# Optimization experiments

Hardware: AMD Instinct MI355X
Metric: run time of the kernel (lower is better)

The kernel has to match this reference:

```python
import jax, jax.numpy as jnp
import numpy as np

N_USERS = 100000
N_MOVIES = 20000
N_EDGES = 600000
FEAT = 64
HID = 128
OUT = 64
N_TUPLES = 100000


def _sage(x_src, x_dst, src_idx, dst_idx, n_dst, Wl, bl, Wr):
    # PyG SAGEConv (mean aggr): lin_l(mean of gathered src feats) + lin_r(x_dst)
    msg = x_src[src_idx]                                        # [E, d_src]
    summ = jax.ops.segment_sum(msg, dst_idx, num_segments=n_dst)
    cnt = jax.ops.segment_sum(jnp.ones((src_idx.shape[0],), x_src.dtype),
                              dst_idx, num_segments=n_dst)
    mean = summ / jnp.maximum(cnt, 1.0)[:, None]
    return mean @ Wl.T + bl + x_dst @ Wr.T


def setup_inputs() -> dict:
    key = jax.random.key(0)
    ks = jax.random.split(key, 20)
    s = 0.05
    return {
        "movie_x": jax.random.normal(ks[0], (N_MOVIES, FEAT), jnp.float32),
        "user_idx": jax.random.randint(ks[1], (N_EDGES,), 0, N_USERS),
        "movie_idx": jax.random.randint(ks[2], (N_EDGES,), 0, N_MOVIES),
        "tuples_coo": jax.random.randint(ks[3], (2, N_TUPLES), 0, N_MOVIES),
        "user_emb": jax.random.normal(ks[4], (1, HID), jnp.float32) * s,
        "W1l": jax.random.normal(ks[5], (HID, FEAT), jnp.float32) * s,
        "b1": jnp.zeros((HID,), jnp.float32),
        "W1r": jax.random.normal(ks[6], (HID, HID), jnp.float32) * s,
        "W2l": jax.random.normal(ks[7], (HID, HID), jnp.float32) * s,
        "b2": jnp.zeros((HID,), jnp.float32),
        "W2r": jax.random.normal(ks[8], (HID, FEAT), jnp.float32) * s,
        "W3l": jax.random.normal(ks[9], (HID, HID), jnp.float32) * s,
        "b3": jnp.zeros((HID,), jnp.float32),
        "W3r": jax.random.normal(ks[10], (HID, HID), jnp.float32) * s,
        "Wlin1": jax.random.normal(ks[11], (OUT, HID), jnp.float32) * s,
        "blin1": jnp.zeros((OUT,), jnp.float32),
        "Wlin2": jax.random.normal(ks[12], (OUT, HID), jnp.float32) * s,
        "blin2": jnp.zeros((OUT,), jnp.float32),
    }


def reference(movie_x, user_idx, movie_idx, tuples_coo, user_emb,
              W1l, b1, W1r, W2l, b2, W2r, W3l, b3, W3r,
              Wlin1, blin1, Wlin2, blin2):
    n_users = N_USERS
    user_x0 = jnp.broadcast_to(user_emb, (n_users, HID))  # emb.weight.repeat
    # conv1: (movie -> user) rev_rates edges: src=movie_idx, dst=user_idx
    user_x = jax.nn.relu(_sage(movie_x, user_x0, movie_idx, user_idx, n_users, W1l, b1, W1r))
    # conv2: (user -> movie) rates edges: src=user_idx, dst=movie_idx
    movie_z = jax.nn.relu(_sage(user_x, movie_x, user_idx, movie_idx, N_MOVIES, W2l, b2, W2r))
    # conv3: (movie -> user) again
    user_z = jax.nn.relu(_sage(movie_z, user_x, movie_idx, user_idx, n_users, W3l, b3, W3r))
    z_user = user_z @ Wlin1.T + blin1
    z_movie = movie_z @ Wlin2.T + blin2
    X = jnp.vstack((z_user, z_movie))
    # relation_schema = ['user', 'movie']: offset movie indices by n_users
    new_index = jnp.vstack((tuples_coo[0], tuples_coo[1] + n_users))
    return X, new_index
```

## Files before the change

### kernel.cpp

```cpp
#include <hip/hip_runtime.h>

typedef __attribute__((ext_vector_type(8))) short short8;
typedef __attribute__((ext_vector_type(4))) float f32x4;

static const int NU = 100000;
static const int NM = 20000;
static const int NE = 600000;
static const int FEAT = 64;
static const int HID = 128;
static const int OUTD = 64;
static const int NTOT = NU + NM;
static const int NLIST = 2 * NE;
static const int CVT_TOT = 81920 + NM * FEAT;
static const int CVT_BLKS = (CVT_TOT + 255) / 256;
static const int IDX_BLKS = (100000 + 255) / 256;

static const int UB_SHIFT = 9;
static const int MB_SHIFT = 7;
static const int NBU = (NU + 511) >> 9;
static const int NBM = (NM + 127) >> 7;
static const int NBUCK = NBU + NBM;
static const int EPB = 4096;
static const int NPBLK = (NE + EPB - 1) / EPB;

__device__ inline float b2f(unsigned short h) {
    unsigned int u = ((unsigned int)h) << 16;
    float f; __builtin_memcpy(&f, &u, 4); return f;
}
__device__ inline unsigned short f2b(float f) {
    unsigned int u; __builtin_memcpy(&u, &f, 4);
    u += 0x7FFFu + ((u >> 16) & 1u);
    return (unsigned short)(u >> 16);
}
__device__ inline unsigned int pk2(float a, float b) {
    return (unsigned int)f2b(a) | ((unsigned int)f2b(b) << 16);
}
__device__ inline int wswz(int row, int bc, int rowbytes) {
    return row * rowbytes + (bc ^ ((row & 7) << 4));
}

__global__ __launch_bounds__(256) void k_hist_misc(
        const int* __restrict__ ui, const int* __restrict__ mi, int* __restrict__ ghist,
        const float* __restrict__ w1l, const float* __restrict__ w2l,
        const float* __restrict__ w2r, const float* __restrict__ w3l,
        const float* __restrict__ w3r, const float* __restrict__ wl1,
        const float* __restrict__ wl2, const float* __restrict__ mx,
        unsigned short* __restrict__ dst,
        const int* __restrict__ tpl, float* __restrict__ oidx,
        const float* __restrict__ ue, const float* __restrict__ w1r,
        const float* __restrict__ b1, float* __restrict__ c1) {
    __shared__ int h[NBUCK];
    const int b = blockIdx.x;
    const int tid = threadIdx.x;
    if (b < NPBLK) {
        for (int i = tid; i < NBUCK; i += 256) h[i] = 0;
        __syncthreads();
#pragma unroll
        for (int it = 0; it < EPB / 256; ++it) {
            int e = b * EPB + it * 256 + tid;
            if (e < NE) {
                atomicAdd(&h[ui[e] >> UB_SHIFT], 1);
                atomicAdd(&h[NBU + (mi[e] >> MB_SHIFT)], 1);
            }
        }
        __syncthreads();
        for (int i = tid; i < NBUCK; i += 256)
            if (h[i]) atomicAdd(&ghist[i], h[i]);
    } else if (b < NPBLK + CVT_BLKS) {
        int g = (b - NPBLK) * 256 + tid;
        if (g >= CVT_TOT) return;
        const float* s; int o;
        if      (g < 8192)   { s = w1l; o = g; }
        else if (g < 24576)  { s = w2l; o = g - 8192; }
        else if (g < 32768)  { s = w2r; o = g - 24576; }
        else if (g < 49152)  { s = w3l; o = g - 32768; }
        else if (g < 65536)  { s = w3r; o = g - 49152; }
        else if (g < 73728)  { s = wl1; o = g - 65536; }
        else if (g < 81920)  { s = wl2; o = g - 73728; }
        else                 { s = mx;  o = g - 81920; }
        dst[g] = f2b(s[o]);
    } else if (b < NPBLK + CVT_BLKS + IDX_BLKS) {
        int i = (b - NPBLK - CVT_BLKS) * 256 + tid;
        if (i < 100000) {
            oidx[i] = (float)tpl[i];
            oidx[100000 + i] = (float)(tpl[100000 + i] + NU);
        }
    } else {
        int hh = tid;
        if (hh < HID) {
            float a = 0.f;
#pragma unroll 16
            for (int k = 0; k < HID; ++k) a += ue[k] * w1r[hh * HID + k];
            c1[hh] = a + b1[hh];
        }
    }
}

__global__ __launch_bounds__(512) void k_bscan(const int* __restrict__ ghist,
                                               int* __restrict__ bb,
                                               int* __restrict__ gcur) {
    __shared__ int s[512];
    const int tid = threadIdx.x;
    int v = (tid < NBUCK) ? ghist[tid] : 0;
    s[tid] = v;
    __syncthreads();
#pragma unroll
    for (int off = 1; off < 512; off <<= 1) {
        int x = (tid >= off) ? s[tid - off] : 0;
        __syncthreads();
        s[tid] += x;
        __syncthreads();
    }
    int excl = s[tid] - v;
    if (tid < NBUCK) { bb[tid] = excl; gcur[tid] = excl; }
    if (tid == 511) bb[NBUCK] = s[511];
}

__global__ __launch_bounds__(256) void k_part(const int* __restrict__ ui,
                                              const int* __restrict__ mi,
                                              int* __restrict__ gcur,
                                              int* __restrict__ entries) {
    __shared__ int h[NBUCK], base[NBUCK], cur[NBUCK];
    const int tid = threadIdx.x;
    for (int i = tid; i < NBUCK; i += 256) h[i] = 0;
    __syncthreads();

    int eu[EPB / 256], em[EPB / 256];
#pragma unroll
    for (int it = 0; it < EPB / 256; ++it) {
        int e = blockIdx.x * EPB + it * 256 + tid;
        if (e < NE) {
            eu[it] = ui[e]; em[it] = mi[e];
            atomicAdd(&h[eu[it] >> UB_SHIFT], 1);
            atomicAdd(&h[NBU + (em[it] >> MB_SHIFT)], 1);
        } else eu[it] = -1;
    }
    __syncthreads();
    for (int i = tid; i < NBUCK; i += 256) {
        int c = h[i];
        base[i] = c ? atomicAdd(&gcur[i], c) : 0;
        cur[i] = 0;
    }
    __syncthreads();
#pragma unroll
    for (int it = 0; it < EPB / 256; ++it) {
        if (eu[it] < 0) continue;
        int u = eu[it], m = em[it];
        int bu = u >> UB_SHIFT;
        int o1 = base[bu] + atomicAdd(&cur[bu], 1);
        entries[o1] = (m << UB_SHIFT) | (u & 511);
        int bm = NBU + (m >> MB_SHIFT);
        int o2 = base[bm] + atomicAdd(&cur[bm], 1);
        entries[o2] = (u << MB_SHIFT) | (m & 127);
    }
}

__global__ __launch_bounds__(256) void k_csr(const int* __restrict__ bb,
                                             const int* __restrict__ entries,
                                             int* __restrict__ rp,
                                             int* __restrict__ list) {
    __shared__ int lcnt[512], lrp[512], lcur[512], ps[256];
    const int b = blockIdx.x;
    const int tid = threadIdx.x;
    const int s = bb[b], e = bb[b + 1];
    const bool isU = b < NBU;
    const int shift = isU ? UB_SHIFT : MB_SHIFT;
    const int mask = isU ? 511 : 127;
    const int n0 = isU ? (b << UB_SHIFT) : ((b - NBU) << MB_SHIFT);
    const int nNodes = isU ? min(512, NU - n0) : min(128, NM - n0);
    const int g0 = isU ? n0 : NU + n0;

    for (int i = tid; i < 512; i += 256) { lcnt[i] = 0; lcur[i] = 0; }
    __syncthreads();
    for (int i = s + tid; i < e; i += 256)
        atomicAdd(&lcnt[entries[i] & mask], 1);
    __syncthreads();
    int a0 = lcnt[2 * tid], a1 = lcnt[2 * tid + 1];
    int pr = a0 + a1;
    ps[tid] = pr;
    __syncthreads();
#pragma unroll
    for (int off = 1; off < 256; off <<= 1) {
        int x = (tid >= off) ? ps[tid - off] : 0;
        __syncthreads();
        ps[tid] += x;
        __syncthreads();
    }
    int excl = ps[tid] - pr;
    lrp[2 * tid] = excl;
    lrp[2 * tid + 1] = excl + a0;
    __syncthreads();
    for (int i = tid; i < nNodes; i += 256) rp[g0 + i] = s + lrp[i];
    if (b == NBUCK - 1 && tid == 0) rp[NTOT] = e;
    for (int i = s + tid; i < e; i += 256) {
        int p = entries[i];
        int dl = p & mask;
        int off = s + lrp[dl] + atomicAdd(&lcur[dl], 1);
        list[off] = p >> shift;
    }
}

template<int C>
__global__ __launch_bounds__(256) void k_gather_b(const unsigned short* __restrict__ src,
                                                  const int* __restrict__ rp,
                                                  const int* __restrict__ list,
                                                  unsigned short* __restrict__ dst,
                                                  int base, int n) {
    constexpr int TPN = C / 8;
    constexpr int NPB = 256 / TPN;
    const int node = blockIdx.x * NPB + threadIdx.x / TPN;
    if (node >= n) return;
    const int c8 = (threadIdx.x % TPN) * 8;
    const int g = base + node;
    const int s = rp[g], e = rp[g + 1];

    float a[8];
#pragma unroll
    for (int j = 0; j < 8; ++j) a[j] = 0.f;

    int i = s;
    for (; i + 1 < e; i += 2) {
        int r0 = list[i], r1 = list[i + 1];
        short8 v0 = *reinterpret_cast<const short8*>(src + (size_t)r0 * C + c8);
        short8 v1 = *reinterpret_cast<const short8*>(src + (size_t)r1 * C + c8);
#pragma unroll
        for (int j = 0; j < 8; ++j)
            a[j] += b2f((unsigned short)v0[j]) + b2f((unsigned short)v1[j]);
    }
    if (i < e) {
        int r0 = list[i];
        short8 v0 = *reinterpret_cast<const short8*>(src + (size_t)r0 * C + c8);
#pragma unroll
        for (int j = 0; j < 8; ++j) a[j] += b2f((unsigned short)v0[j]);
    }
    const float sc = 1.0f / (float)max(e - s, 1);
    short8 o;
#pragma unroll
    for (int j = 0; j < 8; ++j) o[j] = (short)f2b(a[j] * sc);
    *reinterpret_cast<short8*>(dst + (size_t)node * C + c8) = o;
}

__global__ __launch_bounds__(256) void k_gather_relu(const unsigned short* __restrict__ Y1,
                                                     const int* __restrict__ rp,
                                                     const int* __restrict__ list,
                                                     const float* __restrict__ c1,
                                                     unsigned short* __restrict__ user_x,
                                                     int n) {
    const int node = blockIdx.x * 16 + threadIdx.x / 16;
    if (node >= n) return;
    const int c8 = (threadIdx.x % 16) * 8;
    const int s = rp[node], e = rp[node + 1];

    float a[8];
#pragma unroll
    for (int j = 0; j < 8; ++j) a[j] = 0.f;

    int i = s;
    for (; i + 1 < e; i += 2) {
        int r0 = list[i], r1 = list[i + 1];
        short8 v0 = *reinterpret_cast<const short8*>(Y1 + (size_t)r0 * HID + c8);
        short8 v1 = *reinterpret_cast<const short8*>(Y1 + (size_t)r1 * HID + c8);
#pragma unroll
        for (int j = 0; j < 8; ++j)
            a[j] += b2f((unsigned short)v0[j]) + b2f((unsigned short)v1[j]);
    }
    if (i < e) {
        int r0 = list[i];
        short8 v0 = *reinterpret_cast<const short8*>(Y1 + (size_t)r0 * HID + c8);
#pragma unroll
        for (int j = 0; j < 8; ++j) a[j] += b2f((unsigned short)v0[j]);
    }
    const float sc = 1.0f / (float)max(e - s, 1);
    float4 cv0 = *reinterpret_cast<const float4*>(c1 + c8);
    float4 cv1 = *reinterpret_cast<const float4*>(c1 + c8 + 4);
    float r[8];
    r[0] = fmaxf(a[0] * sc + cv0.x, 0.f); r[1] = fmaxf(a[1] * sc + cv0.y, 0.f);
    r[2] = fmaxf(a[2] * sc + cv0.z, 0.f); r[3] = fmaxf(a[3] * sc + cv0.w, 0.f);
    r[4] = fmaxf(a[4] * sc + cv1.x, 0.f); r[5] = fmaxf(a[5] * sc + cv1.y, 0.f);
    r[6] = fmaxf(a[6] * sc + cv1.z, 0.f); r[7] = fmaxf(a[7] * sc + cv1.w, 0.f);
    uint4 o;
    o.x = pk2(r[0], r[1]); o.y = pk2(r[2], r[3]);
    o.z = pk2(r[4], r[5]); o.w = pk2(r[6], r[7]);
    *reinterpret_cast<uint4*>(user_x + (size_t)node * HID + c8) = o;
}

template<int K, int NO, bool AVEC, bool RELU, bool F32OUT>
__global__ __launch_bounds__(256) void k_mf2(const unsigned short* __restrict__ X,
                                             const unsigned short* __restrict__ W,
                                             const float* __restrict__ vec,
                                             void* __restrict__ Yv, int M) {
    constexpr int KT = K / 32;
    constexpr int CG = NO / 16;
    constexpr int WB = NO * K * 2;
    constexpr int RB = K * 2;
    __shared__ __align__(16) char lds[WB];
    const int tid = threadIdx.x;
    const int lane = tid & 63;
    const int wv = tid >> 6;
    const int rbase = blockIdx.x * 128 + wv * 32;
    const int lr = lane & 15;
    const int kg = lane >> 4;

#pragma unroll
    for (int i = 0; i < WB / 16 / 256; ++i) {
        int idx = tid + i * 256;
        int row = idx / (RB / 16);
        int bc = (idx % (RB / 16)) * 16;
        *reinterpret_cast<uint4*>(lds + wswz(row, bc, RB)) =
            *reinterpret_cast<const uint4*>((const char*)W + idx * 16);
    }

    short8 xb[2][KT];
#pragma unroll
    for (int t = 0; t < 2; ++t) {
        int row = min(rbase + t * 16 + lr, M - 1);
#pragma unroll
        for (int kt = 0; kt < KT; ++kt)
            xb[t][kt] = *reinterpret_cast<const short8*>(
                X + (size_t)row * K + kt * 32 + kg * 8);
    }
    __syncthreads();

    f32x4 acc[2][CG];
#pragma unroll
    for (int t = 0; t < 2; ++t)
#pragma unroll
        for (int c = 0; c < CG; ++c) acc[t][c] = (f32x4){0.f, 0.f, 0.f, 0.f};

#pragma unroll
    for (int cg = 0; cg < CG; ++cg) {
        short8 wf[KT];
#pragma unroll
        for (int kt = 0; kt < KT; ++kt)
            wf[kt] = *reinterpret_cast<const short8*>(
                lds + wswz(cg * 16 + lr, kt * 64 + kg * 16, RB));
#pragma unroll
        for (int kt = 0; kt < KT; ++kt)
#pragma unroll
            for (int t = 0; t < 2; ++t)
                acc[t][cg] = __builtin_amdgcn_mfma_f32_16x16x32_bf16(
                    wf[kt], xb[t][kt], acc[t][cg], 0, 0, 0);
    }

#pragma unroll
    for (int t = 0; t < 2; ++t) {
        const int u = rbase + t * 16 + lr;
        if (u >= M) continue;
#pragma unroll
        for (int cg = 0; cg < CG; ++cg) {
            const int h0 = cg * 16 + kg * 4;
            float v[4];
#pragma unroll
            for (int r = 0; r < 4; ++r) v[r] = acc[t][cg][r];
            if (AVEC) {
                float4 vv = *reinterpret_cast<const float4*>(vec + h0);
                v[0] += vv.x; v[1] += vv.y; v[2] += vv.z; v[3] += vv.w;
            }
            if (RELU)
#pragma unroll
                for (int r = 0; r < 4; ++r) v[r] = fmaxf(v[r], 0.f);
            if (F32OUT) {
                float4 o = make_float4(v[0], v[1], v[2], v[3]);
                *reinterpret_cast<float4*>((float*)Yv + (size_t)u * NO + h0) = o;
            } else {
                uint2 o = make_uint2(pk2(v[0], v[1]), pk2(v[2], v[3]));
                *reinterpret_cast<uint2*>((unsigned short*)Yv + (size_t)u * NO + h0) = o;
            }
        }
    }
}

__global__ __launch_bounds__(256) void k_fused_u(
        const unsigned short* __restrict__ S3, const unsigned short* __restrict__ user_x,
        const unsigned short* __restrict__ W3r, const float* __restrict__ b3,
        const unsigned short* __restrict__ Wl1, const float* __restrict__ bl1,
        float* __restrict__ out, int M) {
    __shared__ __align__(16) char lds[49152];
    const int tid = threadIdx.x;
    const int lane = tid & 63;
    const int wv = tid >> 6;
    const int rbase = blockIdx.x * 128 + wv * 32;
    const int lr = lane & 15;
    const int kg = lane >> 4;

#pragma unroll
    for (int i = 0; i < 8; ++i) {
        int idx = tid + i * 256;
        int row = idx >> 4, bc = (idx & 15) << 4;
        *reinterpret_cast<uint4*>(lds + wswz(row, bc, 256)) =
            *reinterpret_cast<const uint4*>((const char*)W3r + idx * 16);
    }
#pragma unroll
    for (int i = 0; i < 4; ++i) {
        int idx = tid + i * 256;
        int row = idx >> 4, bc = (idx & 15) << 4;
        *reinterpret_cast<uint4*>(lds + 32768 + wswz(row, bc, 256)) =
            *reinterpret_cast<const uint4*>((const char*)Wl1 + idx * 16);
    }

    short8 xc[2][4];
#pragma unroll
    for (int t = 0; t < 2; ++t) {
        int row = min(rbase + t * 16 + lr, M - 1);
#pragma unroll
        for (int kt = 0; kt < 4; ++kt)
            xc[t][kt] = *reinterpret_cast<const short8*>(
                user_x + (size_t)row * HID + kt * 32 + kg * 8);
    }
    __syncthreads();

    f32x4 acc[2][8];
#pragma unroll
    for (int t = 0; t < 2; ++t)
#pragma unroll
        for (int c = 0; c < 8; ++c) acc[t][c] = (f32x4){0.f, 0.f, 0.f, 0.f};

#pragma unroll
    for (int cg = 0; cg < 8; ++cg) {
        short8 wr[4];
#pragma unroll
        for (int kt = 0; kt < 4; ++kt)
            wr[kt] = *reinterpret_cast<const short8*>(
                lds + wswz(cg * 16 + lr, kt * 64 + kg * 16, 256));
#pragma unroll
        for (int kt = 0; kt < 4; ++kt)
#pragma unroll
            for (int t = 0; t < 2; ++t)
                acc[t][cg] = __builtin_amdgcn_mfma_f32_16x16x32_bf16(
                    wr[kt], xc[t][kt], acc[t][cg], 0, 0, 0);
    }
    __syncthreads();

#pragma unroll
    for (int t = 0; t < 2; ++t) {
        const int ul = wv * 32 + t * 16 + lr;
        const int u = min(rbase + t * 16 + lr, M - 1);
#pragma unroll
        for (int cg = 0; cg < 8; ++cg) {
            const int h0 = cg * 16 + kg * 4;
            uint2 s3 = *reinterpret_cast<const uint2*>(S3 + (size_t)u * HID + h0);
            float4 vv = *reinterpret_cast<const float4*>(b3 + h0);
            float v0 = fmaxf(acc[t][cg][0] + b2f((unsigned short)(s3.x & 0xffff)) + vv.x, 0.f);
            float v1 = fmaxf(acc[t][cg][1] + b2f((unsigned short)(s3.x >> 16)) + vv.y, 0.f);
            float v2 = fmaxf(acc[t][cg][2] + b2f((unsigned short)(s3.y & 0xffff)) + vv.z, 0.f);
            float v3 = fmaxf(acc[t][cg][3] + b2f((unsigned short)(s3.y >> 16)) + vv.w, 0.f);
            uint2 pk = make_uint2(pk2(v0, v1), pk2(v2, v3));
            *reinterpret_cast<uint2*>(lds + wswz(ul, h0 * 2, 256)) = pk;
        }
    }
    __syncthreads();

    short8 zb[2][4];
#pragma unroll
    for (int t = 0; t < 2; ++t) {
        const int ul = wv * 32 + t * 16 + lr;
#pragma unroll
        for (int kt = 0; kt < 4; ++kt)
            zb[t][kt] = *reinterpret_cast<const short8*>(
                lds + wswz(ul, kt * 64 + kg * 16, 256));
    }
    f32x4 a2[2][4];
#pragma unroll
    for (int t = 0; t < 2; ++t)
#pragma unroll
        for (int c = 0; c < 4; ++c) a2[t][c] = (f32x4){0.f, 0.f, 0.f, 0.f};
#pragma unroll
    for (int cg = 0; cg < 4; ++cg) {
        short8 wf[4];
#pragma unroll
        for (int kt = 0; kt < 4; ++kt)
            wf[kt] = *reinterpret_cast<const short8*>(
                lds + 32768 + wswz(cg * 16 + lr, kt * 64 + kg * 16, 256));
#pragma unroll
        for (int kt = 0; kt < 4; ++kt)
#pragma unroll
            for (int t = 0; t < 2; ++t)
                a2[t][cg] = __builtin_amdgcn_mfma_f32_16x16x32_bf16(
                    wf[kt], zb[t][kt], a2[t][cg], 0, 0, 0);
    }
#pragma unroll
    for (int t = 0; t < 2; ++t) {
        const int u = rbase + t * 16 + lr;
        if (u >= M) continue;
#pragma unroll
        for (int cg = 0; cg < 4; ++cg) {
            const int o0 = cg * 16 + kg * 4;
            float4 bb = *reinterpret_cast<const float4*>(bl1 + o0);
            float4 o = make_float4(a2[t][cg][0] + bb.x, a2[t][cg][1] + bb.y,
                                   a2[t][cg][2] + bb.z, a2[t][cg][3] + bb.w);
            *reinterpret_cast<float4*>(out + (size_t)u * OUTD + o0) = o;
        }
    }
}

__global__ __launch_bounds__(256) void k_fused_m(
        const unsigned short* __restrict__ mean2, const unsigned short* __restrict__ mxb,
        const unsigned short* __restrict__ W2l, const unsigned short* __restrict__ W2r,
        const float* __restrict__ b2, unsigned short* __restrict__ movie_z,
        const unsigned short* __restrict__ Wl2, const float* __restrict__ bl2,
        const unsigned short* __restrict__ W3l, unsigned short* __restrict__ Y3,
        float* __restrict__ out, int M) {
    __shared__ __align__(16) char lds[65536];
    const int tid = threadIdx.x;
    const int lane = tid & 63;
    const int wv = tid >> 6;
    const int rbase = blockIdx.x * 128 + wv * 32;
    const int lr = lane & 15;
    const int kg = lane >> 4;

#pragma unroll
    for (int i = 0; i < 8; ++i) {
        int idx = tid + i * 256;
        int row = idx >> 4, bc = (idx & 15) << 4;
        *reinterpret_cast<uint4*>(lds + wswz(row, bc, 256)) =
            *reinterpret_cast<const uint4*>((const char*)W2l + idx * 16);
    }
#pragma unroll
    for (int i = 0; i < 4; ++i) {
        int idx = tid + i * 256;
        int row = idx >> 3, bc = (idx & 7) << 4;
        *reinterpret_cast<uint4*>(lds + 32768 + wswz(row, bc, 128)) =
            *reinterpret_cast<const uint4*>((const char*)W2r + idx * 16);
        int row2 = idx >> 4, bc2 = (idx & 15) << 4;
        *reinterpret_cast<uint4*>(lds + 49152 + wswz(row2, bc2, 256)) =
            *reinterpret_cast<const uint4*>((const char*)Wl2 + idx * 16);
    }

    short8 xa[2][4], xc[2][2];
#pragma unroll
    for (int t = 0; t < 2; ++t) {
        int row = min(rbase + t * 16 + lr, M - 1);
#pragma unroll
        for (int kt = 0; kt < 4; ++kt)
            xa[t][kt] = *reinterpret_cast<const short8*>(
                mean2 + (size_t)row * HID + kt * 32 + kg * 8);
#pragma unroll
        for (int kt = 0; kt < 2; ++kt)
            xc[t][kt] = *reinterpret_cast<const short8*>(
                mxb + (size_t)row * FEAT + kt * 32 + kg * 8);
    }
    __syncthreads();

    f32x4 acc[2][8];
#pragma unroll
    for (int t = 0; t < 2; ++t)
#pragma unroll
        for (int c = 0; c < 8; ++c) acc[t][c] = (f32x4){0.f, 0.f, 0.f, 0.f};

#pragma unroll
    for (int cg = 0; cg < 8; ++cg) {
        short8 wl[4], wr[2];
#pragma unroll
        for (int kt = 0; kt < 4; ++kt)
            wl[kt] = *reinterpret_cast<const short8*>(
                lds + wswz(cg * 16 + lr, kt * 64 + kg * 16, 256));
#pragma unroll
        for (int kt = 0; kt < 2; ++kt)
            wr[kt] = *reinterpret_cast<const short8*>(
                lds + 32768 + wswz(cg * 16 + lr, kt * 64 + kg * 16, 128));
#pragma unroll
        for (int kt = 0; kt < 4; ++kt)
#pragma unroll
            for (int t = 0; t < 2; ++t)
                acc[t][cg] = __builtin_amdgcn_mfma_f32_16x16x32_bf16(
                    wl[kt], xa[t][kt], acc[t][cg], 0, 0, 0);
#pragma unroll
        for (int kt = 0; kt < 2; ++kt)
#pragma unroll
            for (int t = 0; t < 2; ++t)
                acc[t][cg] = __builtin_amdgcn_mfma_f32_16x16x32_bf16(
                    wr[kt], xc[t][kt], acc[t][cg], 0, 0, 0);
    }
    __syncthreads();

#pragma unroll
    for (int t = 0; t < 2; ++t) {
        const int ul = wv * 32 + t * 16 + lr;
        const int u = rbase + t * 16 + lr;
#pragma unroll
        for (int cg = 0; cg < 8; ++cg) {
            const int h0 = cg * 16 + kg * 4;
            float4 vv = *reinterpret_cast<const float4*>(b2 + h0);
            float v0 = fmaxf(acc[t][cg][0] + vv.x, 0.f);
            float v1 = fmaxf(acc[t][cg][1] + vv.y, 0.f);
            float v2 = fmaxf(acc[t][cg][2] + vv.z, 0.f);
            float v3 = fmaxf(acc[t][cg][3] + vv.w, 0.f);
            uint2 pk = make_uint2(pk2(v0, v1), pk2(v2, v3));
            *reinterpret_cast<uint2*>(lds + wswz(ul, h0 * 2, 256)) = pk;
            if (u < M)
                *reinterpret_cast<uint2*>(movie_z + (size_t)u * HID + h0) = pk;
        }
    }
    __syncthreads();

    short8 zb[2][4];
#pragma unroll
    for (int t = 0; t < 2; ++t) {
        const int ul = wv * 32 + t * 16 + lr;
#pragma unroll
        for (int kt = 0; kt < 4; ++kt)
            zb[t][kt] = *reinterpret_cast<const short8*>(
                lds + wswz(ul, kt * 64 + kg * 16, 256));
    }
    f32x4 a2[2][4];
#pragma unroll
    for (int t = 0; t < 2; ++t)
#pragma unroll
        for (int c = 0; c < 4; ++c) a2[t][c] = (f32x4){0.f, 0.f, 0.f, 0.f};
#pragma unroll
    for (int cg = 0; cg < 4; ++cg) {
        short8 wf[4];
#pragma unroll
        for (int kt = 0; kt < 4; ++kt)
            wf[kt] = *reinterpret_cast<const short8*>(
                lds + 49152 + wswz(cg * 16 + lr, kt * 64 + kg * 16, 256));
#pragma unroll
        for (int kt = 0; kt < 4; ++kt)
#pragma unroll
            for (int t = 0; t < 2; ++t)
                a2[t][cg] = __builtin_amdgcn_mfma_f32_16x16x32_bf16(
                    wf[kt], zb[t][kt], a2[t][cg], 0, 0, 0);
    }
#pragma unroll
    for (int t = 0; t < 2; ++t) {
        const int u = rbase + t * 16 + lr;
        if (u >= M) continue;
#pragma unroll
        for (int cg = 0; cg < 4; ++cg) {
            const int o0 = cg * 16 + kg * 4;
            float4 bb = *reinterpret_cast<const float4*>(bl2 + o0);
            float4 o = make_float4(a2[t][cg][0] + bb.x, a2[t][cg][1] + bb.y,
                                   a2[t][cg][2] + bb.z, a2[t][cg][3] + bb.w);
            *reinterpret_cast<float4*>(out + (size_t)u * OUTD + o0) = o;
        }
    }
    __syncthreads();

#pragma unroll
    for (int i = 0; i < 8; ++i) {
        int idx = tid + i * 256;
        int row = idx >> 4, bc = (idx & 15) << 4;
        *reinterpret_cast<uint4*>(lds + 32768 + wswz(row, bc, 256)) =
            *reinterpret_cast<const uint4*>((const char*)W3l + idx * 16);
    }
    __syncthreads();

    f32x4 a3[2][8];
#pragma unroll
    for (int t = 0; t < 2; ++t)
#pragma unroll
        for (int c = 0; c < 8; ++c) a3[t][c] = (f32x4){0.f, 0.f, 0.f, 0.f};
#pragma unroll
    for (int cg = 0; cg < 8; ++cg) {
        short8 wf[4];
#pragma unroll
        for (int kt = 0; kt < 4; ++kt)
            wf[kt] = *reinterpret_cast<const short8*>(
                lds + 32768 + wswz(cg * 16 + lr, kt * 64 + kg * 16, 256));
#pragma unroll
        for (int kt = 0; kt < 4; ++kt)
#pragma unroll
            for (int t = 0; t < 2; ++t)
                a3[t][cg] = __builtin_amdgcn_mfma_f32_16x16x32_bf16(
                    wf[kt], zb[t][kt], a3[t][cg], 0, 0, 0);
    }
#pragma unroll
    for (int t = 0; t < 2; ++t) {
        const int u = rbase + t * 16 + lr;
        if (u >= M) continue;
#pragma unroll
        for (int cg = 0; cg < 8; ++cg) {
            const int h0 = cg * 16 + kg * 4;
            uint2 pk = make_uint2(pk2(a3[t][cg][0], a3[t][cg][1]),
                                  pk2(a3[t][cg][2], a3[t][cg][3]));
            *reinterpret_cast<uint2*>(Y3 + (size_t)u * HID + h0) = pk;
        }
    }
}

extern "C" void kernel_launch(void* const* d_in, const int* in_sizes, int n_in,
                              void* d_out, int out_size, void* d_ws, size_t ws_size,
                              hipStream_t stream) {
    const float* movie_x  = (const float*)d_in[0];
    const int*   user_idx = (const int*)d_in[1];
    const int*   movie_idx= (const int*)d_in[2];
    const int*   tuples   = (const int*)d_in[3];
    const float* user_emb = (const float*)d_in[4];
    const float* W1l = (const float*)d_in[5];
    const float* b1  = (const float*)d_in[6];
    const float* W1r = (const float*)d_in[7];
    const float* W2l = (const float*)d_in[8];
    const float* b2  = (const float*)d_in[9];
    const float* W2r = (const float*)d_in[10];
    const float* W3l = (const float*)d_in[11];
    const float* b3  = (const float*)d_in[12];
    const float* W3r = (const float*)d_in[13];
    const float* Wlin1 = (const float*)d_in[14];
    const float* blin1 = (const float*)d_in[15];
    const float* Wlin2 = (const float*)d_in[16];
    const float* blin2 = (const float*)d_in[17];

    float* out = (float*)d_out;

    char* p = (char*)d_ws;
    int* ghist = (int*)p;  p += 360 * 4;
    int* bb    = (int*)p;  p += 360 * 4;
    int* gcur  = (int*)p;  p += 360 * 4;
    int* entries = (int*)p; p += (size_t)NLIST * 4;
    int* rp    = (int*)p;  p += (size_t)(NTOT + 8) * 4;
    int* list  = (int*)p;  p += (size_t)NLIST * 4;
    float* c1  = (float*)p; p += 128 * 4;
    unsigned short* wb = (unsigned short*)p; p += (size_t)CVT_TOT * 2;
    unsigned short* W1l_b  = wb;
    unsigned short* W2l_b  = wb + 8192;
    unsigned short* W2r_b  = wb + 24576;
    unsigned short* W3l_b  = wb + 32768;
    unsigned short* W3r_b  = wb + 49152;
    unsigned short* Wlin1_b= wb + 65536;
    unsigned short* Wlin2_b= wb + 73728;
    unsigned short* mxb    = wb + 81920;
    unsigned short* Y1     = (unsigned short*)p; p += (size_t)NM * HID * 2;
    unsigned short* user_x = (unsigned short*)p; p += (size_t)NU * HID * 2;
    unsigned short* mean2  = (unsigned short*)p; p += (size_t)NM * HID * 2;
    unsigned short* movie_z= (unsigned short*)p; p += (size_t)NM * HID * 2;
    unsigned short* Y3     = (unsigned short*)p; p += (size_t)NM * HID * 2;
    unsigned short* S3     = (unsigned short*)p; p += (size_t)NU * HID * 2;

    hipMemsetAsync(ghist, 0, NBUCK * sizeof(int), stream);
    k_hist_misc<<<NPBLK + CVT_BLKS + IDX_BLKS + 1, 256, 0, stream>>>(
        user_idx, movie_idx, ghist,
        W1l, W2l, W2r, W3l, W3r, Wlin1, Wlin2, movie_x, wb,
        tuples, out + (size_t)(NU + NM) * OUTD, user_emb, W1r, b1, c1);
    k_mf2<FEAT, HID, false, false, false><<<(NM + 127) / 128, 256, 0, stream>>>(
        mxb, W1l_b, nullptr, Y1, NM);
    k_bscan<<<1, 512, 0, stream>>>(ghist, bb, gcur);
    k_part<<<NPBLK, 256, 0, stream>>>(user_idx, movie_idx, gcur, entries);
    k_csr<<<NBUCK, 256, 0, stream>>>(bb, entries, rp, list);

    k_gather_relu<<<(NU + 15) / 16, 256, 0, stream>>>(Y1, rp, list, c1, user_x, NU);

    k_gather_b<HID><<<(NM + 15) / 16, 256, 0, stream>>>(user_x, rp, list, mean2, NU, NM);
    k_fused_m<<<(NM + 127) / 128, 256, 0, stream>>>(
        mean2, mxb, W2l_b, W2r_b, b2, movie_z, Wlin2_b, blin2, W3l_b, Y3,
        out + (size_t)NU * OUTD, NM);

    k_gather_b<HID><<<(NU + 15) / 16, 256, 0, stream>>>(Y3, rp, list, S3, 0, NU);
    k_fused_u<<<(NU + 127) / 128, 256, 0, stream>>>(
        S3, user_x, W3r_b, b3, Wlin1_b, blin1, out, NU);
}
```

Measured before the change: 166.8 us.

## Replace bucket histogram+scan with fixed-capacity bucket slots and start/end row pointers

Drops the global histogram, single-block scan and separate partition kernel by giving every bucket a fixed CAP-sized slot, so partitioning happens in the first fused kernel with atomics per bucket. CSR row pointers become (start,end) int2 pairs because the list is no longer contiguous. The gather loops are also unrolled from 2 to 4 neighbours for more memory-level parallelism. This assumes no bucket exceeds 8192 entries (about 3072 expected for user buckets, 3840 for movie buckets), and it enlarges the workspace while saving two launches.

```diff
diff --git a/kernel.cpp b/kernel.cpp
--- a/kernel.cpp
+++ b/kernel.cpp
@@ -10,7 +10,6 @@
 static const int HID = 128;
 static const int OUTD = 64;
 static const int NTOT = NU + NM;
-static const int NLIST = 2 * NE;
 static const int CVT_TOT = 81920 + NM * FEAT;
 static const int CVT_BLKS = (CVT_TOT + 255) / 256;
 static const int IDX_BLKS = (100000 + 255) / 256;
@@ -22,6 +21,7 @@
 static const int NBUCK = NBU + NBM;
 static const int EPB = 4096;
 static const int NPBLK = (NE + EPB - 1) / EPB;
+static const int CAP = 8192;
 
 __device__ inline float b2f(unsigned short h) {
     unsigned int u = ((unsigned int)h) << 16;
@@ -39,8 +39,9 @@
     return row * rowbytes + (bc ^ ((row & 7) << 4));
 }
 
-__global__ __launch_bounds__(256) void k_hist_misc(
-        const int* __restrict__ ui, const int* __restrict__ mi, int* __restrict__ ghist,
+__global__ __launch_bounds__(256) void k_part_misc(
+        const int* __restrict__ ui, const int* __restrict__ mi,
+        int* __restrict__ gcur, int* __restrict__ entries,
         const float* __restrict__ w1l, const float* __restrict__ w2l,
         const float* __restrict__ w2r, const float* __restrict__ w3l,
         const float* __restrict__ w3r, const float* __restrict__ wl1,
@@ -49,23 +50,40 @@
         const int* __restrict__ tpl, float* __restrict__ oidx,
         const float* __restrict__ ue, const float* __restrict__ w1r,
         const float* __restrict__ b1, float* __restrict__ c1) {
-    __shared__ int h[NBUCK];
+    __shared__ int h[NBUCK], base[NBUCK], cur[NBUCK];
     const int b = blockIdx.x;
     const int tid = threadIdx.x;
     if (b < NPBLK) {
         for (int i = tid; i < NBUCK; i += 256) h[i] = 0;
         __syncthreads();
+        int eu[EPB / 256], em[EPB / 256];
 #pragma unroll
         for (int it = 0; it < EPB / 256; ++it) {
             int e = b * EPB + it * 256 + tid;
             if (e < NE) {
-                atomicAdd(&h[ui[e] >> UB_SHIFT], 1);
-                atomicAdd(&h[NBU + (mi[e] >> MB_SHIFT)], 1);
-            }
+                eu[it] = ui[e]; em[it] = mi[e];
+                atomicAdd(&h[eu[it] >> UB_SHIFT], 1);
+                atomicAdd(&h[NBU + (em[it] >> MB_SHIFT)], 1);
+            } else eu[it] = -1;
         }
         __syncthreads();
-        for (int i = tid; i < NBUCK; i += 256)
-            if (h[i]) atomicAdd(&ghist[i], h[i]);
+        for (int i = tid; i < NBUCK; i += 256) {
+            int c = h[i];
+            base[i] = c ? (i * CAP + atomicAdd(&gcur[i], c)) : 0;
+            cur[i] = 0;
+        }
+        __syncthreads();
+#pragma unroll
+        for (int it = 0; it < EPB / 256; ++it) {
+            if (eu[it] < 0) continue;
+            int u = eu[it], m = em[it];
+            int bu = u >> UB_SHIFT;
+            int o1 = base[bu] + atomicAdd(&cur[bu], 1);
+            entries[o1] = (m << UB_SHIFT) | (u & 511);
+            int bm = NBU + (m >> MB_SHIFT);
+            int o2 = base[bm] + atomicAdd(&cur[bm], 1);
+            entries[o2] = (u << MB_SHIFT) | (m & 127);
+        }
     } else if (b < NPBLK + CVT_BLKS) {
         int g = (b - NPBLK) * 256 + tid;
         if (g >= CVT_TOT) return;
@@ -96,73 +114,15 @@
     }
 }
 
-__global__ __launch_bounds__(512) void k_bscan(const int* __restrict__ ghist,
-                                               int* __restrict__ bb,
-                                               int* __restrict__ gcur) {
-    __shared__ int s[512];
-    const int tid = threadIdx.x;
-    int v = (tid < NBUCK) ? ghist[tid] : 0;
-    s[tid] = v;
-    __syncthreads();
-#pragma unroll
-    for (int off = 1; off < 512; off <<= 1) {
-        int x = (tid >= off) ? s[tid - off] : 0;
-        __syncthreads();
-        s[tid] += x;
-        __syncthreads();
-    }
-    int excl = s[tid] - v;
-    if (tid < NBUCK) { bb[tid] = excl; gcur[tid] = excl; }
-    if (tid == 511) bb[NBUCK] = s[511];
-}
-
-__global__ __launch_bounds__(256) void k_part(const int* __restrict__ ui,
-                                              const int* __restrict__ mi,
-                                              int* __restrict__ gcur,
-                                              int* __restrict__ entries) {
-    __shared__ int h[NBUCK], base[NBUCK], cur[NBUCK];
-    const int tid = threadIdx.x;
-    for (int i = tid; i < NBUCK; i += 256) h[i] = 0;
-    __syncthreads();
-
-    int eu[EPB / 256], em[EPB / 256];
-#pragma unroll
-    for (int it = 0; it < EPB / 256; ++it) {
-        int e = blockIdx.x * EPB + it * 256 + tid;
-        if (e < NE) {
-            eu[it] = ui[e]; em[it] = mi[e];
-            atomicAdd(&h[eu[it] >> UB_SHIFT], 1);
-            atomicAdd(&h[NBU + (em[it] >> MB_SHIFT)], 1);
-        } else eu[it] = -1;
-    }
-    __syncthreads();
-    for (int i = tid; i < NBUCK; i += 256) {
-        int c = h[i];
-        base[i] = c ? atomicAdd(&gcur[i], c) : 0;
-        cur[i] = 0;
-    }
-    __syncthreads();
-#pragma unroll
-    for (int it = 0; it < EPB / 256; ++it) {
-        if (eu[it] < 0) continue;
-        int u = eu[it], m = em[it];
-        int bu = u >> UB_SHIFT;
-        int o1 = base[bu] + atomicAdd(&cur[bu], 1);
-        entries[o1] = (m << UB_SHIFT) | (u & 511);
-        int bm = NBU + (m >> MB_SHIFT);
-        int o2 = base[bm] + atomicAdd(&cur[bm], 1);
-        entries[o2] = (u << MB_SHIFT) | (m & 127);
-    }
-}
-
-__global__ __launch_bounds__(256) void k_csr(const int* __restrict__ bb,
+__global__ __launch_bounds__(256) void k_csr(const int* __restrict__ gcur,
                                              const int* __restrict__ entries,
-                                             int* __restrict__ rp,
+                                             int2* __restrict__ rp2,
                                              int* __restrict__ list) {
     __shared__ int lcnt[512], lrp[512], lcur[512], ps[256];
     const int b = blockIdx.x;
     const int tid = threadIdx.x;
-    const int s = bb[b], e = bb[b + 1];
+    const int s = b * CAP;
+    const int e = s + gcur[b];
     const bool isU = b < NBU;
     const int shift = isU ? UB_SHIFT : MB_SHIFT;
     const int mask = isU ? 511 : 127;
@@ -190,8 +150,8 @@
     lrp[2 * tid] = excl;
     lrp[2 * tid + 1] = excl + a0;
     __syncthreads();
-    for (int i = tid; i < nNodes; i += 256) rp[g0 + i] = s + lrp[i];
-    if (b == NBUCK - 1 && tid == 0) rp[NTOT] = e;
+    for (int i = tid; i < nNodes; i += 256)
+        rp2[g0 + i] = make_int2(s + lrp[i], s + lrp[i] + lcnt[i]);
     for (int i = s + tid; i < e; i += 256) {
         int p = entries[i];
         int dl = p & mask;
@@ -202,7 +162,7 @@
 
 template<int C>
 __global__ __launch_bounds__(256) void k_gather_b(const unsigned short* __restrict__ src,
-                                                  const int* __restrict__ rp,
+                                                  const int2* __restrict__ rp2,
                                                   const int* __restrict__ list,
                                                   unsigned short* __restrict__ dst,
                                                   int base, int n) {
@@ -211,23 +171,26 @@
     const int node = blockIdx.x * NPB + threadIdx.x / TPN;
     if (node >= n) return;
     const int c8 = (threadIdx.x % TPN) * 8;
-    const int g = base + node;
-    const int s = rp[g], e = rp[g + 1];
+    const int2 se = rp2[base + node];
+    const int s = se.x, e = se.y;
 
     float a[8];
 #pragma unroll
     for (int j = 0; j < 8; ++j) a[j] = 0.f;
 
     int i = s;
-    for (; i + 1 < e; i += 2) {
-        int r0 = list[i], r1 = list[i + 1];
+    for (; i + 3 < e; i += 4) {
+        int r0 = list[i], r1 = list[i + 1], r2 = list[i + 2], r3 = list[i + 3];
         short8 v0 = *reinterpret_cast<const short8*>(src + (size_t)r0 * C + c8);
         short8 v1 = *reinterpret_cast<const short8*>(src + (size_t)r1 * C + c8);
+        short8 v2 = *reinterpret_cast<const short8*>(src + (size_t)r2 * C + c8);
+        short8 v3 = *reinterpret_cast<const short8*>(src + (size_t)r3 * C + c8);
 #pragma unroll
         for (int j = 0; j < 8; ++j)
-            a[j] += b2f((unsigned short)v0[j]) + b2f((unsigned short)v1[j]);
-    }
-    if (i < e) {
+            a[j] += (b2f((unsigned short)v0[j]) + b2f((unsigned short)v1[j]))
+                  + (b2f((unsigned short)v2[j]) + b2f((unsigned short)v3[j]));
+    }
+    for (; i < e; ++i) {
         int r0 = list[i];
         short8 v0 = *reinterpret_cast<const short8*>(src + (size_t)r0 * C + c8);
 #pragma unroll
@@ -241,7 +204,7 @@
 }
 
 __global__ __launch_bounds__(256) void k_gather_relu(const unsigned short* __restrict__ Y1,
-                                                     const int* __restrict__ rp,
+                                                     const int2* __restrict__ rp2,
                                                      const int* __restrict__ list,
                                                      const float* __restrict__ c1,
                                                      unsigned short* __restrict__ user_x,
@@ -249,22 +212,26 @@
     const int node = blockIdx.x * 16 + threadIdx.x / 16;
     if (node >= n) return;
     const int c8 = (threadIdx.x % 16) * 8;
-    const int s = rp[node], e = rp[node + 1];
+    const int2 se = rp2[node];
+    const int s = se.x, e = se.y;
 
     float a[8];
 #pragma unroll
     for (int j = 0; j < 8; ++j) a[j] = 0.f;
 
     int i = s;
-    for (; i + 1 < e; i += 2) {
-        int r0 = list[i], r1 = list[i + 1];
+    for (; i + 3 < e; i += 4) {
+        int r0 = list[i], r1 = list[i + 1], r2 = list[i + 2], r3 = list[i + 3];
         short8 v0 = *reinterpret_cast<const short8*>(Y1 + (size_t)r0 * HID + c8);
         short8 v1 = *reinterpret_cast<const short8*>(Y1 + (size_t)r1 * HID + c8);
+        short8 v2 = *reinterpret_cast<const short8*>(Y1 + (size_t)r2 * HID + c8);
+        short8 v3 = *reinterpret_cast<const short8*>(Y1 + (size_t)r3 * HID + c8);
 #pragma unroll
         for (int j = 0; j < 8; ++j)
-            a[j] += b2f((unsigned short)v0[j]) + b2f((unsigned short)v1[j]);
-    }
-    if (i < e) {
+            a[j] += (b2f((unsigned short)v0[j]) + b2f((unsigned short)v1[j]))
+                  + (b2f((unsigned short)v2[j]) + b2f((unsigned short)v3[j]));
+    }
+    for (; i < e; ++i) {
         int r0 = list[i];
         short8 v0 = *reinterpret_cast<const short8*>(Y1 + (size_t)r0 * HID + c8);
 #pragma unroll
@@ -703,12 +670,10 @@
     float* out = (float*)d_out;
 
     char* p = (char*)d_ws;
-    int* ghist = (int*)p;  p += 360 * 4;
-    int* bb    = (int*)p;  p += 360 * 4;
-    int* gcur  = (int*)p;  p += 360 * 4;
-    int* entries = (int*)p; p += (size_t)NLIST * 4;
-    int* rp    = (int*)p;  p += (size_t)(NTOT + 8) * 4;
-    int* list  = (int*)p;  p += (size_t)NLIST * 4;
+    int* gcur = (int*)p;  p += 360 * 4;
+    int* entries = (int*)p; p += (size_t)NBUCK * CAP * 4;
+    int2* rp2  = (int2*)p; p += (size_t)NTOT * 8;
+    int* list  = (int*)p;  p += (size_t)NBUCK * CAP * 4;
     float* c1  = (float*)p; p += 128 * 4;
     unsigned short* wb = (unsigned short*)p; p += (size_t)CVT_TOT * 2;
     unsigned short* W1l_b  = wb;
@@ -726,25 +691,23 @@
     unsigned short* Y3     = (unsigned short*)p; p += (size_t)NM * HID * 2;
     unsigned short* S3     = (unsigned short*)p; p += (size_t)NU * HID * 2;
 
-    hipMemsetAsync(ghist, 0, NBUCK * sizeof(int), stream);
-    k_hist_misc<<<NPBLK + CVT_BLKS + IDX_BLKS + 1, 256, 0, stream>>>(
-        user_idx, movie_idx, ghist,
+    hipMemsetAsync(gcur, 0, NBUCK * sizeof(int), stream);
+    k_part_misc<<<NPBLK + CVT_BLKS + IDX_BLKS + 1, 256, 0, stream>>>(
+        user_idx, movie_idx, gcur, entries,
         W1l, W2l, W2r, W3l, W3r, Wlin1, Wlin2, movie_x, wb,
         tuples, out + (size_t)(NU + NM) * OUTD, user_emb, W1r, b1, c1);
+    k_csr<<<NBUCK, 256, 0, stream>>>(gcur, entries, rp2, list);
     k_mf2<FEAT, HID, false, false, false><<<(NM + 127) / 128, 256, 0, stream>>>(
         mxb, W1l_b, nullptr, Y1, NM);
-    k_bscan<<<1, 512, 0, stream>>>(ghist, bb, gcur);
-    k_part<<<NPBLK, 256, 0, stream>>>(user_idx, movie_idx, gcur, entries);
-    k_csr<<<NBUCK, 256, 0, stream>>>(bb, entries, rp, list);
-
-    k_gather_relu<<<(NU + 15) / 16, 256, 0, stream>>>(Y1, rp, list, c1, user_x, NU);
-
-    k_gather_b<HID><<<(NM + 15) / 16, 256, 0, stream>>>(user_x, rp, list, mean2, NU, NM);
+
+    k_gather_relu<<<(NU + 15) / 16, 256, 0, stream>>>(Y1, rp2, list, c1, user_x, NU);
+
+    k_gather_b<HID><<<(NM + 15) / 16, 256, 0, stream>>>(user_x, rp2, list, mean2, NU, NM);
     k_fused_m<<<(NM + 127) / 128, 256, 0, stream>>>(
         mean2, mxb, W2l_b, W2r_b, b2, movie_z, Wlin2_b, blin2, W3l_b, Y3,
         out + (size_t)NU * OUTD, NM);
 
-    k_gather_b<HID><<<(NU + 15) / 16, 256, 0, stream>>>(Y3, rp, list, S3, 0, NU);
+    k_gather_b<HID><<<(NU + 15) / 16, 256, 0, stream>>>(Y3, rp2, list, S3, 0, NU);
     k_fused_u<<<(NU + 127) / 128, 256, 0, stream>>>(
         S3, user_x, W3r_b, b3, Wlin1_b, blin1, out, NU);
 }
```

Measured after the change: 164.2 us. About the same (-1.5%).
